# Optimization experiments

Measured on AMD Instinct MI355X. Metric: run time of the kernel, lower is better.

Reference implementation:

```python
import jax, jax.numpy as jnp
import numpy as np

EPS = 1e-5
H = 8  # num_heads

def ln(x, g, b):
    m = x.mean(-1, keepdims=True)
    v = ((x - m) ** 2).mean(-1, keepdims=True)
    return (x - m) / jnp.sqrt(v + EPS) * g + b

def gca(qf, kf, p):
    # Gated cross-modal attention (eval mode, dropout off, mask all-True => no mask)
    (nqg, nqb, nkg, nkb, wq, bq, wk, bk, wv, bv, wo, bo,
     wgp, bgp, g1w, g1b, glng, glnb, g2w, g2b) = p
    B, Sq, _ = qf.shape
    Sk = kf.shape[1]
    E = wq.shape[1]
    D = E // H
    qn = ln(qf, nqg, nqb)
    kn = ln(kf, nkg, nkb)
    q = (qn @ wq + bq).reshape(B, Sq, H, D)
    k = (kn @ wk + bk).reshape(B, Sk, H, D)
    v = (kn @ wv + bv).reshape(B, Sk, H, D)
    scores = jnp.einsum('bqhd,bkhd->bhqk', q, k) * (D ** -0.5)
    w = jax.nn.softmax(scores, axis=-1)          # [B,H,Sq,Sk]
    ctx = jnp.einsum('bhqk,bkhd->bqhd', w, v).reshape(B, Sq, E)
    att = ctx @ wo + bo                          # cross-attention output
    qp = qf @ wgp + bgp                          # query projected for gating
    h = jnp.concatenate([qp, att], axis=-1) @ g1w + g1b
    gate = jax.nn.sigmoid(jax.nn.gelu(ln(h, glng, glnb), approximate=False) @ g2w + g2b)
    return qp + gate * att, w

def ff(x, lng, lnb, w1, b1, w2, b2):
    y = jax.nn.gelu(ln(x, lng, lnb) @ w1 + b1, approximate=False)
    return x + (y @ w2 + b2)

def setup_inputs() -> dict:
    B, Sv, St, Vd, Td, F = 8, 1024, 512, 1024, 768, 512
    keys = iter(jax.random.split(jax.random.key(0), 80))
    def nrm(shape):
        return jax.random.normal(next(keys), shape, jnp.float32) * 0.02
    d = {}
    d['vision_features'] = jax.random.normal(next(keys), (B, Sv, Vd), jnp.float32)
    d['text_features'] = jax.random.normal(next(keys), (B, St, Td), jnp.float32)
    def attn_params(pfx, qd, kd, e):
        d[pfx + 'nq_g'] = jnp.ones(qd); d[pfx + 'nq_b'] = jnp.zeros(qd)
        d[pfx + 'nk_g'] = jnp.ones(kd); d[pfx + 'nk_b'] = jnp.zeros(kd)
        d[pfx + 'wq'] = nrm((qd, e)); d[pfx + 'bq'] = jnp.zeros(e)
        d[pfx + 'wk'] = nrm((kd, e)); d[pfx + 'bk'] = jnp.zeros(e)
        d[pfx + 'wv'] = nrm((kd, e)); d[pfx + 'bv'] = jnp.zeros(e)
        d[pfx + 'wo'] = nrm((e, e)); d[pfx + 'bo'] = jnp.zeros(e)
        d[pfx + 'wgp'] = nrm((qd, e)); d[pfx + 'bgp'] = jnp.zeros(e)
        d[pfx + 'g1w'] = nrm((2 * e, e)); d[pfx + 'g1b'] = jnp.zeros(e)
        d[pfx + 'glng'] = jnp.ones(e); d[pfx + 'glnb'] = jnp.zeros(e)
        d[pfx + 'g2w'] = nrm((e, e)); d[pfx + 'g2b'] = jnp.zeros(e)
    attn_params('t2v_', Td, Vd, F)  # text queries attend to vision
    attn_params('v2t_', Vd, Td, F)  # vision queries attend to text
    for pfx in ('vff_', 'tff_'):
        d[pfx + 'lng'] = jnp.ones(F); d[pfx + 'lnb'] = jnp.zeros(F)
        d[pfx + 'w1'] = nrm((F, 4 * F)); d[pfx + 'b1'] = jnp.zeros(4 * F)
        d[pfx + 'w2'] = nrm((4 * F, F)); d[pfx + 'b2'] = jnp.zeros(F)
    return d

def reference(vision_features, text_features,
              t2v_nq_g, t2v_nq_b, t2v_nk_g, t2v_nk_b, t2v_wq, t2v_bq, t2v_wk, t2v_bk, t2v_wv, t2v_bv, t2v_wo, t2v_bo, t2v_wgp, t2v_bgp, t2v_g1w, t2v_g1b, t2v_glng, t2v_glnb, t2v_g2w, t2v_g2b,
              v2t_nq_g, v2t_nq_b, v2t_nk_g, v2t_nk_b, v2t_wq, v2t_bq, v2t_wk, v2t_bk, v2t_wv, v2t_bv, v2t_wo, v2t_bo, v2t_wgp, v2t_bgp, v2t_g1w, v2t_g1b, v2t_glng, v2t_glnb, v2t_g2w, v2t_g2b,
              vff_lng, vff_lnb, vff_w1, vff_b1, vff_w2, vff_b2,
              tff_lng, tff_lnb, tff_w1, tff_b1, tff_w2, tff_b2):
    t2v_p = (t2v_nq_g, t2v_nq_b, t2v_nk_g, t2v_nk_b, t2v_wq, t2v_bq, t2v_wk, t2v_bk, t2v_wv, t2v_bv, t2v_wo, t2v_bo, t2v_wgp, t2v_bgp, t2v_g1w, t2v_g1b, t2v_glng, t2v_glnb, t2v_g2w, t2v_g2b)
    v2t_p = (v2t_nq_g, v2t_nq_b, v2t_nk_g, v2t_nk_b, v2t_wq, v2t_bq, v2t_wk, v2t_bk, v2t_wv, v2t_bv, v2t_wo, v2t_bo, v2t_wgp, v2t_bgp, v2t_g1w, v2t_g1b, v2t_glng, v2t_glnb, v2t_g2w, v2t_g2b)
    text_att, t2v_w = gca(text_features, vision_features, t2v_p)
    vis_att, v2t_w = gca(vision_features, text_features, v2t_p)
    vision_out = ff(vis_att, vff_lng, vff_lnb, vff_w1, vff_b1, vff_w2, vff_b2)
    text_out = ff(text_att, tff_lng, tff_lnb, tff_w1, tff_b1, tff_w2, tff_b2)
    return (vision_out, text_out, t2v_w, v2t_w)
```

## Files before the change

kernel.cpp:

```cpp
#include <hip/hip_runtime.h>
#include <math.h>


typedef __attribute__((ext_vector_type(8))) short s16x8;
typedef __attribute__((ext_vector_type(4))) float f32x4;
typedef __attribute__((ext_vector_type(4))) unsigned short us4;

__device__ __forceinline__ float gelu_exact(float x) {
  return 0.5f * x * (1.0f + erff(x * 0.70710678118654752f));
}
__device__ __forceinline__ float sigmoidf_(float x) {
  return 1.0f / (1.0f + expf(-x));
}
__device__ __forceinline__ unsigned short f2bf(float f) {
  unsigned int u = __float_as_uint(f);
  u += 0x7fffu + ((u >> 16) & 1u);
  return (unsigned short)(u >> 16);
}

template <bool GELU>
__global__ __launch_bounds__(256) void ln_kernel(
    const float* __restrict__ x, const float* __restrict__ g,
    const float* __restrict__ b, unsigned short* __restrict__ out, int cols) {
  const int row = blockIdx.x;
  const float2* xr = (const float2*)(x + (size_t)row * cols);
  const float2* g2 = (const float2*)g;
  const float2* b2 = (const float2*)b;
  const int n2 = cols >> 1;
  const int tid = threadIdx.x;
  float s = 0.f, ss = 0.f;
  for (int c = tid; c < n2; c += 256) {
    float2 v = xr[c];
    s += v.x + v.y;
    ss += v.x * v.x + v.y * v.y;
  }
#pragma unroll
  for (int off = 32; off; off >>= 1) {
    s += __shfl_down(s, off, 64);
    ss += __shfl_down(ss, off, 64);
  }
  __shared__ float rs[4], rss[4], stat[2];
  const int lane = tid & 63, wid = tid >> 6;
  if (lane == 0) {
    rs[wid] = s;
    rss[wid] = ss;
  }
  __syncthreads();
  if (tid == 0) {
    float ts = rs[0] + rs[1] + rs[2] + rs[3];
    float tss = rss[0] + rss[1] + rss[2] + rss[3];
    float m = ts / (float)cols;
    float var = tss / (float)cols - m * m;
    stat[0] = m;
    stat[1] = 1.0f / sqrtf(var + 1e-5f);
  }
  __syncthreads();
  const float m = stat[0], inv = stat[1];
  ushort2* o2 = (ushort2*)(out + (size_t)row * cols);
  for (int c = tid; c < n2; c += 256) {
    float2 v = xr[c];
    float2 gg = g2[c], bb = b2[c];
    float o0 = (v.x - m) * inv * gg.x + bb.x;
    float o1 = (v.y - m) * inv * gg.y + bb.y;
    if (GELU) {
      o0 = gelu_exact(o0);
      o1 = gelu_exact(o1);
    }
    ushort2 r;
    r.x = f2bf(o0);
    r.y = f2bf(o1);
    o2[c] = r;
  }
}

template <int NIT>
__global__ __launch_bounds__(256) void softmax_kernel(
    float* __restrict__ p, unsigned short* __restrict__ pb) {
  const size_t base = (size_t)blockIdx.x * (NIT * 512);
  float2* pr = (float2*)(p + base);
  ushort2* pb2 = (ushort2*)(pb + base);
  const int tid = threadIdx.x;
  float2 vals[NIT];
  float mx = -1e30f;
#pragma unroll
  for (int i = 0; i < NIT; ++i) {
    vals[i] = pr[tid + i * 256];
    mx = fmaxf(mx, fmaxf(vals[i].x, vals[i].y));
  }
  __shared__ float red[4];
#pragma unroll
  for (int off = 32; off; off >>= 1) mx = fmaxf(mx, __shfl_down(mx, off, 64));
  const int lane = tid & 63, wid = tid >> 6;
  if (lane == 0) red[wid] = mx;
  __syncthreads();
  mx = fmaxf(fmaxf(red[0], red[1]), fmaxf(red[2], red[3]));
  float s = 0.f;
#pragma unroll
  for (int i = 0; i < NIT; ++i) {
    vals[i].x = expf(vals[i].x - mx);
    vals[i].y = expf(vals[i].y - mx);
    s += vals[i].x + vals[i].y;
  }
  __syncthreads();
#pragma unroll
  for (int off = 32; off; off >>= 1) s += __shfl_down(s, off, 64);
  if (lane == 0) red[wid] = s;
  __syncthreads();
  s = red[0] + red[1] + red[2] + red[3];
  const float inv = 1.0f / s;
#pragma unroll
  for (int i = 0; i < NIT; ++i) {
    float2 o;
    o.x = vals[i].x * inv;
    o.y = vals[i].y * inv;
    pr[tid + i * 256] = o;
    ushort2 r;
    r.x = f2bf(o.x);
    r.y = f2bf(o.y);
    pb2[tid + i * 256] = r;
  }
}

__global__ __launch_bounds__(256) void cast_kernel(
    const float* __restrict__ x, unsigned short* __restrict__ o, int n4) {
  const int stride = gridDim.x * 256;
  for (int i = blockIdx.x * 256 + threadIdx.x; i < n4; i += stride) {
    float4 v = ((const float4*)x)[i];
    us4 r = {f2bf(v.x), f2bf(v.y), f2bf(v.z), f2bf(v.w)};
    ((us4*)o)[i] = r;
  }
}

struct TP {
  const float* s[8];
  unsigned short* d[8];
};
__global__ __launch_bounds__(256) void tc_kernel(TP tp, int R, int C) {
  __shared__ unsigned short tile[32][33];
  const float* src = tp.s[blockIdx.z];
  unsigned short* dst = tp.d[blockIdx.z];
  const int r0 = blockIdx.y * 32, c0 = blockIdx.x * 32;
  const int t = threadIdx.x;
  const int tr = t >> 3, tc4 = (t & 7) * 4;
  float4 v = *(const float4*)(src + (size_t)(r0 + tr) * C + c0 + tc4);
  tile[tr][tc4 + 0] = f2bf(v.x);
  tile[tr][tc4 + 1] = f2bf(v.y);
  tile[tr][tc4 + 2] = f2bf(v.z);
  tile[tr][tc4 + 3] = f2bf(v.w);
  __syncthreads();
  us4 o = {tile[tc4 + 0][tr], tile[tc4 + 1][tr], tile[tc4 + 2][tr],
           tile[tc4 + 3][tr]};
  *(us4*)(dst + (size_t)(c0 + tr) * R + r0 + tc4) = o;
}

enum { EPI_B = 0, EPI_BG = 1, EPI_BR = 2, EPI_BGATE = 3, EPI_SC = 4 };

template <int ROWS>
__device__ __forceinline__ void stage_tile(unsigned short (*lds)[40],
                                           const unsigned short* __restrict__ g,
                                           size_t ld) {
  const int t = threadIdx.x;
  const int jr = t & 3;
  const int B0 = (jr < 2) ? (jr * 32) : ((jr - 2) * 32 + 8);
#pragma unroll
  for (int p = 0; p < ROWS / 64; ++p) {
    const int row = (t >> 2) + p * 64;
    uint4 u = *(const uint4*)(g + (size_t)row * ld + jr * 8);
    char* dst = (char*)(&lds[row][0]) + B0;
    *(unsigned long long*)dst = ((const unsigned long long*)&u)[0];
    *(unsigned long long*)(dst + 16) = ((const unsigned long long*)&u)[1];
  }
}

template <int EPI, int OM, int BN, bool CONCAT>
__global__ __launch_bounds__(256) void mm(
    const unsigned short* __restrict__ A0,
    const unsigned short* __restrict__ A1, int lda0, int lda1, int K0, int K,
    const unsigned short* __restrict__ Bt, int ldb,
    const float* __restrict__ bias, const float* __restrict__ X1,
    const float* __restrict__ X2, float* __restrict__ outF,
    unsigned short* __restrict__ outB, int ldc, float scale, size_t aZb,
    size_t aZh, size_t bZb, size_t bZh, size_t cZb, size_t cZh) {
  constexpr int WN = BN / 2;
  constexpr int NJ = WN / 16;
  __shared__ unsigned short As[128][40];
  __shared__ unsigned short Bs[BN][40];
  const int z = blockIdx.z;
  const size_t zb = z >> 3, zh = z & 7;
  const int m0 = blockIdx.y * 128, n0 = blockIdx.x * BN;
  const int t = threadIdx.x;
  const int w = t >> 6, lane = t & 63;
  const int h = lane >> 4, r16 = lane & 15;
  const int wm = w >> 1, wn = w & 1;
  const unsigned short* Ab = A0 + zb * aZb + zh * aZh + (size_t)m0 * lda0;
  const unsigned short* A1b = CONCAT ? (A1 + (size_t)m0 * lda1) : nullptr;
  const unsigned short* Bb = Bt + zb * bZb + zh * bZh + (size_t)n0 * ldb;
  f32x4 acc[4][NJ] = {};
  for (int k0 = 0; k0 < K; k0 += 32) {
    const unsigned short* ag;
    size_t lda;
    if (CONCAT && k0 >= K0) {
      ag = A1b + (k0 - K0);
      lda = (size_t)lda1;
    } else {
      ag = Ab + k0;
      lda = (size_t)lda0;
    }
    stage_tile<128>(As, ag, lda);
    stage_tile<BN>(Bs, Bb + k0, (size_t)ldb);
    __syncthreads();
    const unsigned short* ap = &As[wm * 64 + r16][h * 8];
    const unsigned short* bp = &Bs[wn * WN + r16][h * 8];
    s16x8 av[4], bv[NJ];
#pragma unroll
    for (int i = 0; i < 4; ++i) av[i] = *(const s16x8*)(ap + i * 640);
#pragma unroll
    for (int j = 0; j < NJ; ++j) bv[j] = *(const s16x8*)(bp + j * 640);
#pragma unroll
    for (int i = 0; i < 4; ++i)
#pragma unroll
      for (int j = 0; j < NJ; ++j)
        acc[i][j] = __builtin_amdgcn_mfma_f32_16x16x32_bf16(av[i], bv[j],
                                                            acc[i][j], 0, 0, 0);
    __syncthreads();
  }
  const size_t cz = zb * cZb + zh * cZh;
#pragma unroll
  for (int i = 0; i < 4; ++i) {
    const int rr = m0 + wm * 64 + i * 16 + h * 4;
#pragma unroll
    for (int j = 0; j < NJ; ++j) {
      const int cc = n0 + wn * WN + j * 16 + r16;
      const float bb = (EPI == EPI_SC) ? 0.f : bias[cc];
#pragma unroll
      for (int q = 0; q < 4; ++q) {
        float v = acc[i][j][q];
        v = (EPI == EPI_SC) ? v * scale : v + bb;
        if (EPI == EPI_BG) v = gelu_exact(v);
        const size_t idx = cz + (size_t)(rr + q) * ldc + cc;
        if (EPI == EPI_BR) v = X1[idx] + v;
        if (EPI == EPI_BGATE) v = X1[idx] + sigmoidf_(v) * X2[idx];
        if (OM & 1) outF[idx] = v;
        if (OM & 2) outB[idx] = f2bf(v);
      }
    }
  }
}

extern "C" void kernel_launch(void* const* d_in, const int* in_sizes, int n_in,
                              void* d_out, int out_size, void* d_ws,
                              size_t ws_size, hipStream_t stream) {
  (void)in_sizes;
  (void)n_in;
  (void)out_size;
  (void)ws_size;
  const int B = 8, Sv = 1024, St = 512, Vd = 1024, Td = 768, E = 512;
  auto inf = [&](int i) { return (const float*)d_in[i]; };
  float* out = (float*)d_out;
  char* ws = (char*)d_ws;
  float* out_vis = out;
  float* out_txt = out + 4194304;
  float* w_t2v = out + 6291456;
  float* w_v2t = out + 39845888;

  const size_t BIGo = 0;
  const size_t R1o = 67108864;
  const size_t R2o = R1o + 16777216;
  const size_t R3o = R2o + 16777216;
  const size_t R4o = R3o + 5767168;
  auto U = [&](size_t o) { return (unsigned short*)(ws + o); };
  auto F = [&](size_t o) { return (float*)(ws + o); };

  {
    const int pb = 2;
    const int Sq = St, Sk = Sv, Mq = B * Sq, Mk = B * Sk;
    unsigned short* wq_t = U(R3o + 0);
    unsigned short* wk_t = U(R3o + 786432);
    unsigned short* wv_t = U(R3o + 1835008);
    unsigned short* wo_t = U(R3o + 2883584);
    unsigned short* wgp_t = U(R3o + 3407872);
    unsigned short* g1w_t = U(R3o + 4194304);
    unsigned short* g2w_t = U(R3o + 5242880);
    {
      TP tp{};
      tp.s[0] = inf(pb + 4); tp.d[0] = wq_t;
      tp.s[1] = inf(pb + 12); tp.d[1] = wgp_t;
      tc_kernel<<<dim3(16, 24, 2), 256, 0, stream>>>(tp, 768, 512);
    }
    {
      TP tp{};
      tp.s[0] = inf(pb + 6); tp.d[0] = wk_t;
      tp.s[1] = inf(pb + 8); tp.d[1] = wv_t;
      tp.s[2] = inf(pb + 14); tp.d[2] = g1w_t;
      tc_kernel<<<dim3(16, 32, 3), 256, 0, stream>>>(tp, 1024, 512);
    }
    {
      TP tp{};
      tp.s[0] = inf(pb + 10); tp.d[0] = wo_t;
      tp.s[1] = inf(pb + 18); tp.d[1] = g2w_t;
      tc_kernel<<<dim3(16, 16, 2), 256, 0, stream>>>(tp, 512, 512);
    }
    unsigned short* qn = U(BIGo);
    unsigned short* kn = U(R1o);
    unsigned short* q_bf = U(BIGo + 16777216);
    unsigned short* k_bf = U(BIGo + 25165824);
    float* v_f = F(R2o);
    unsigned short* w_bf = U(BIGo);
    unsigned short* vt = U(R4o);
    unsigned short* ctx_bf = U(R1o);
    float* att_f = F(R2o);
    unsigned short* att_bf = U(BIGo + 50331648);
    unsigned short* txt_bf = U(BIGo);
    float* qp_f = F(R1o + 8388608);
    unsigned short* qp_bf = U(BIGo + 58720256);
    float* h_f = F(BIGo + 16777216);
    unsigned short* hg = U(BIGo);

    ln_kernel<false><<<Mq, 256, 0, stream>>>(inf(1), inf(pb + 0), inf(pb + 1),
                                             qn, Td);
    ln_kernel<false><<<Mk, 256, 0, stream>>>(inf(0), inf(pb + 2), inf(pb + 3),
                                             kn, Vd);
    mm<EPI_B, 2, 64, false><<<dim3(8, 32, 1), 256, 0, stream>>>(
        qn, nullptr, Td, 0, Td, Td, wq_t, Td, inf(pb + 5), nullptr, nullptr,
        nullptr, q_bf, E, 1.f, 0, 0, 0, 0, 0, 0);
    mm<EPI_B, 2, 128, false><<<dim3(4, 64, 1), 256, 0, stream>>>(
        kn, nullptr, Vd, 0, Vd, Vd, wk_t, Vd, inf(pb + 7), nullptr, nullptr,
        nullptr, k_bf, E, 1.f, 0, 0, 0, 0, 0, 0);
    mm<EPI_B, 1, 128, false><<<dim3(4, 64, 1), 256, 0, stream>>>(
        kn, nullptr, Vd, 0, Vd, Vd, wv_t, Vd, inf(pb + 9), nullptr, nullptr,
        v_f, nullptr, E, 1.f, 0, 0, 0, 0, 0, 0);
    mm<EPI_SC, 1, 128, false><<<dim3(Sk / 128, Sq / 128, 64), 256, 0, stream>>>(
        q_bf, nullptr, E, 0, 64, 64, k_bf, E, nullptr, nullptr, nullptr,
        w_t2v, nullptr, Sk, 0.125f, (size_t)Sq * E, 64, (size_t)Sk * E, 64,
        (size_t)8 * Sq * Sk, (size_t)Sq * Sk);
    softmax_kernel<2><<<64 * Sq, 256, 0, stream>>>(w_t2v, w_bf);
    {
      TP tp{};
      for (int i = 0; i < 8; ++i) {
        tp.s[i] = v_f + (size_t)i * Sk * E;
        tp.d[i] = vt + (size_t)i * E * Sk;
      }
      tc_kernel<<<dim3(E / 32, Sk / 32, 8), 256, 0, stream>>>(tp, Sk, E);
    }
    mm<EPI_SC, 2, 64, false><<<dim3(1, Sq / 128, 64), 256, 0, stream>>>(
        w_bf, nullptr, Sk, 0, Sk, Sk, vt, Sk, nullptr, nullptr, nullptr,
        nullptr, ctx_bf, E, 1.f, (size_t)8 * Sq * Sk, (size_t)Sq * Sk,
        (size_t)E * Sk, (size_t)64 * Sk, (size_t)Sq * E, 64);
    mm<EPI_B, 3, 64, false><<<dim3(8, 32, 1), 256, 0, stream>>>(
        ctx_bf, nullptr, E, 0, E, E, wo_t, E, inf(pb + 11), nullptr, nullptr,
        att_f, att_bf, E, 1.f, 0, 0, 0, 0, 0, 0);
    cast_kernel<<<1024, 256, 0, stream>>>(inf(1), txt_bf, Mq * Td / 4);
    mm<EPI_B, 3, 64, false><<<dim3(8, 32, 1), 256, 0, stream>>>(
        txt_bf, nullptr, Td, 0, Td, Td, wgp_t, Td, inf(pb + 13), nullptr,
        nullptr, qp_f, qp_bf, E, 1.f, 0, 0, 0, 0, 0, 0);
    mm<EPI_B, 1, 64, true><<<dim3(8, 32, 1), 256, 0, stream>>>(
        qp_bf, att_bf, E, E, E, 2 * E, g1w_t, 2 * E, inf(pb + 15), nullptr,
        nullptr, h_f, nullptr, E, 1.f, 0, 0, 0, 0, 0, 0);
    ln_kernel<true><<<Mq, 256, 0, stream>>>(h_f, inf(pb + 16), inf(pb + 17),
                                            hg, E);
    mm<EPI_BGATE, 1, 64, false><<<dim3(8, 32, 1), 256, 0, stream>>>(
        hg, nullptr, E, 0, E, E, g2w_t, E, inf(pb + 19), qp_f, att_f, out_txt,
        nullptr, E, 1.f, 0, 0, 0, 0, 0, 0);
  }
  {
    const int pb = 22;
    const int Sq = Sv, Sk = St, Mq = B * Sq, Mk = B * Sk;
    unsigned short* wq_t = U(R3o + 0);
    unsigned short* wk_t = U(R3o + 1048576);
    unsigned short* wv_t = U(R3o + 1835008);
    unsigned short* wo_t = U(R3o + 2621440);
    unsigned short* wgp_t = U(R3o + 3145728);
    unsigned short* g1w_t = U(R3o + 4194304);
    unsigned short* g2w_t = U(R3o + 5242880);
    {
      TP tp{};
      tp.s[0] = inf(pb + 4); tp.d[0] = wq_t;
      tp.s[1] = inf(pb + 12); tp.d[1] = wgp_t;
      tp.s[2] = inf(pb + 14); tp.d[2] = g1w_t;
      tc_kernel<<<dim3(16, 32, 3), 256, 0, stream>>>(tp, 1024, 512);
    }
    {
      TP tp{};
      tp.s[0] = inf(pb + 6); tp.d[0] = wk_t;
      tp.s[1] = inf(pb + 8); tp.d[1] = wv_t;
      tc_kernel<<<dim3(16, 24, 2), 256, 0, stream>>>(tp, 768, 512);
    }
    {
      TP tp{};
      tp.s[0] = inf(pb + 10); tp.d[0] = wo_t;
      tp.s[1] = inf(pb + 18); tp.d[1] = g2w_t;
      tc_kernel<<<dim3(16, 16, 2), 256, 0, stream>>>(tp, 512, 512);
    }
    unsigned short* qn = U(BIGo);
    unsigned short* kn = U(R1o);
    unsigned short* q_bf = U(BIGo + 16777216);
    unsigned short* k_bf = U(BIGo + 25165824);
    float* v_f = F(R2o);
    unsigned short* w_bf = U(BIGo);
    unsigned short* vt = U(R4o);
    unsigned short* ctx_bf = U(R1o);
    float* att_f = F(R2o);
    unsigned short* att_bf = U(BIGo + 50331648);
    unsigned short* vis_bf = U(BIGo);
    float* qp_f = F(R1o);
    unsigned short* qp_bf = U(BIGo + 58720256);
    float* h_f = F(BIGo + 16777216);
    unsigned short* hg = U(BIGo);

    ln_kernel<false><<<Mq, 256, 0, stream>>>(inf(0), inf(pb + 0), inf(pb + 1),
                                             qn, Vd);
    ln_kernel<false><<<Mk, 256, 0, stream>>>(inf(1), inf(pb + 2), inf(pb + 3),
                                             kn, Td);
    mm<EPI_B, 2, 128, false><<<dim3(4, 64, 1), 256, 0, stream>>>(
        qn, nullptr, Vd, 0, Vd, Vd, wq_t, Vd, inf(pb + 5), nullptr, nullptr,
        nullptr, q_bf, E, 1.f, 0, 0, 0, 0, 0, 0);
    mm<EPI_B, 2, 64, false><<<dim3(8, 32, 1), 256, 0, stream>>>(
        kn, nullptr, Td, 0, Td, Td, wk_t, Td, inf(pb + 7), nullptr, nullptr,
        nullptr, k_bf, E, 1.f, 0, 0, 0, 0, 0, 0);
    mm<EPI_B, 1, 64, false><<<dim3(8, 32, 1), 256, 0, stream>>>(
        kn, nullptr, Td, 0, Td, Td, wv_t, Td, inf(pb + 9), nullptr, nullptr,
        v_f, nullptr, E, 1.f, 0, 0, 0, 0, 0, 0);
    mm<EPI_SC, 1, 128, false><<<dim3(Sk / 128, Sq / 128, 64), 256, 0, stream>>>(
        q_bf, nullptr, E, 0, 64, 64, k_bf, E, nullptr, nullptr, nullptr,
        w_v2t, nullptr, Sk, 0.125f, (size_t)Sq * E, 64, (size_t)Sk * E, 64,
        (size_t)8 * Sq * Sk, (size_t)Sq * Sk);
    softmax_kernel<1><<<64 * Sq, 256, 0, stream>>>(w_v2t, w_bf);
    {
      TP tp{};
      for (int i = 0; i < 8; ++i) {
        tp.s[i] = v_f + (size_t)i * Sk * E;
        tp.d[i] = vt + (size_t)i * E * Sk;
      }
      tc_kernel<<<dim3(E / 32, Sk / 32, 8), 256, 0, stream>>>(tp, Sk, E);
    }
    mm<EPI_SC, 2, 64, false><<<dim3(1, Sq / 128, 64), 256, 0, stream>>>(
        w_bf, nullptr, Sk, 0, Sk, Sk, vt, Sk, nullptr, nullptr, nullptr,
        nullptr, ctx_bf, E, 1.f, (size_t)8 * Sq * Sk, (size_t)Sq * Sk,
        (size_t)E * Sk, (size_t)64 * Sk, (size_t)Sq * E, 64);
    mm<EPI_B, 3, 128, false><<<dim3(4, 64, 1), 256, 0, stream>>>(
        ctx_bf, nullptr, E, 0, E, E, wo_t, E, inf(pb + 11), nullptr, nullptr,
        att_f, att_bf, E, 1.f, 0, 0, 0, 0, 0, 0);
    cast_kernel<<<2048, 256, 0, stream>>>(inf(0), vis_bf, Mq * Vd / 4);
    mm<EPI_B, 3, 128, false><<<dim3(4, 64, 1), 256, 0, stream>>>(
        vis_bf, nullptr, Vd, 0, Vd, Vd, wgp_t, Vd, inf(pb + 13), nullptr,
        nullptr, qp_f, qp_bf, E, 1.f, 0, 0, 0, 0, 0, 0);
    mm<EPI_B, 1, 128, true><<<dim3(4, 64, 1), 256, 0, stream>>>(
        qp_bf, att_bf, E, E, E, 2 * E, g1w_t, 2 * E, inf(pb + 15), nullptr,
        nullptr, h_f, nullptr, E, 1.f, 0, 0, 0, 0, 0, 0);
    ln_kernel<true><<<Mq, 256, 0, stream>>>(h_f, inf(pb + 16), inf(pb + 17),
                                            hg, E);
    mm<EPI_BGATE, 1, 128, false><<<dim3(4, 64, 1), 256, 0, stream>>>(
        hg, nullptr, E, 0, E, E, g2w_t, E, inf(pb + 19), qp_f, att_f, out_vis,
        nullptr, E, 1.f, 0, 0, 0, 0, 0, 0);
  }
  {
    unsigned short* vw1_t = U(R3o + 0);
    unsigned short* vw2_t = U(R3o + 2097152);
    unsigned short* tw1_t = U(R3o + 4194304);
    unsigned short* tw2_t = U(R3o + 6291456);
    {
      TP tp{};
      tp.s[0] = inf(44); tp.d[0] = vw1_t;
      tp.s[1] = inf(50); tp.d[1] = tw1_t;
      tc_kernel<<<dim3(64, 16, 2), 256, 0, stream>>>(tp, 512, 2048);
    }
    {
      TP tp{};
      tp.s[0] = inf(46); tp.d[0] = vw2_t;
      tp.s[1] = inf(52); tp.d[1] = tw2_t;
      tc_kernel<<<dim3(16, 64, 2), 256, 0, stream>>>(tp, 2048, 512);
    }
    unsigned short* lnv = U(BIGo);
    unsigned short* y_v = U(BIGo + 8388608);
    unsigned short* lnt = U(BIGo + 41943040);
    unsigned short* y_t = U(BIGo + 46137344);
    ln_kernel<false><<<8192, 256, 0, stream>>>(out_vis, inf(42), inf(43), lnv,
                                               512);
    mm<EPI_BG, 2, 128, false><<<dim3(16, 64, 1), 256, 0, stream>>>(
        lnv, nullptr, 512, 0, 512, 512, vw1_t, 512, inf(45), nullptr, nullptr,
        nullptr, y_v, 2048, 1.f, 0, 0, 0, 0, 0, 0);
    mm<EPI_BR, 1, 128, false><<<dim3(4, 64, 1), 256, 0, stream>>>(
        y_v, nullptr, 2048, 0, 2048, 2048, vw2_t, 2048, inf(47), out_vis,
        nullptr, out_vis, nullptr, 512, 1.f, 0, 0, 0, 0, 0, 0);
    ln_kernel<false><<<4096, 256, 0, stream>>>(out_txt, inf(48), inf(49), lnt,
                                               512);
    mm<EPI_BG, 2, 128, false><<<dim3(16, 32, 1), 256, 0, stream>>>(
        lnt, nullptr, 512, 0, 512, 512, tw1_t, 512, inf(51), nullptr, nullptr,
        nullptr, y_t, 2048, 1.f, 0, 0, 0, 0, 0, 0);
    mm<EPI_BR, 1, 64, false><<<dim3(8, 32, 1), 256, 0, stream>>>(
        y_t, nullptr, 2048, 0, 2048, 2048, tw2_t, 2048, inf(53), out_txt,
        nullptr, out_txt, nullptr, 512, 1.f, 0, 0, 0, 0, 0, 0);
  }
}
```

Measured before the change: 1.209 ms.

## Fuse QK scores with softmax and merge K/V projections with transposed V output

Measured after the change: 1.190 ms. Within noise of the previous version (-1.5%).

```diff
diff --git a/kernel.cpp b/kernel.cpp
--- a/kernel.cpp
+++ b/kernel.cpp
@@ -70,54 +70,6 @@
     r.x = f2bf(o0);
     r.y = f2bf(o1);
     o2[c] = r;
-  }
-}
-
-template <int NIT>
-__global__ __launch_bounds__(256) void softmax_kernel(
-    float* __restrict__ p, unsigned short* __restrict__ pb) {
-  const size_t base = (size_t)blockIdx.x * (NIT * 512);
-  float2* pr = (float2*)(p + base);
-  ushort2* pb2 = (ushort2*)(pb + base);
-  const int tid = threadIdx.x;
-  float2 vals[NIT];
-  float mx = -1e30f;
-#pragma unroll
-  for (int i = 0; i < NIT; ++i) {
-    vals[i] = pr[tid + i * 256];
-    mx = fmaxf(mx, fmaxf(vals[i].x, vals[i].y));
-  }
-  __shared__ float red[4];
-#pragma unroll
-  for (int off = 32; off; off >>= 1) mx = fmaxf(mx, __shfl_down(mx, off, 64));
-  const int lane = tid & 63, wid = tid >> 6;
-  if (lane == 0) red[wid] = mx;
-  __syncthreads();
-  mx = fmaxf(fmaxf(red[0], red[1]), fmaxf(red[2], red[3]));
-  float s = 0.f;
-#pragma unroll
-  for (int i = 0; i < NIT; ++i) {
-    vals[i].x = expf(vals[i].x - mx);
-    vals[i].y = expf(vals[i].y - mx);
-    s += vals[i].x + vals[i].y;
-  }
-  __syncthreads();
-#pragma unroll
-  for (int off = 32; off; off >>= 1) s += __shfl_down(s, off, 64);
-  if (lane == 0) red[wid] = s;
-  __syncthreads();
-  s = red[0] + red[1] + red[2] + red[3];
-  const float inv = 1.0f / s;
-#pragma unroll
-  for (int i = 0; i < NIT; ++i) {
-    float2 o;
-    o.x = vals[i].x * inv;
-    o.y = vals[i].y * inv;
-    pr[tid + i * 256] = o;
-    ushort2 r;
-    r.x = f2bf(o.x);
-    r.y = f2bf(o.y);
-    pb2[tid + i * 256] = r;
   }
 }
 
@@ -153,7 +105,107 @@
   *(us4*)(dst + (size_t)(c0 + tr) * R + r0 + tc4) = o;
 }
 
-enum { EPI_B = 0, EPI_BG = 1, EPI_BR = 2, EPI_BGATE = 3, EPI_SC = 4 };
+template <int SK>
+__global__ __launch_bounds__(256) void attn_sm(
+    const unsigned short* __restrict__ qp, const unsigned short* __restrict__ kp,
+    float* __restrict__ w, unsigned short* __restrict__ wb, int Sq,
+    float scale) {
+  constexpr int TPW = SK / 64;
+  const int z = blockIdx.y, b = z >> 3, h = z & 7;
+  const int q0 = blockIdx.x * 16;
+  const int t = threadIdx.x, wv = t >> 6, lane = t & 63;
+  const int hh = lane >> 4, r16 = lane & 15;
+  const unsigned short* qrow =
+      qp + (size_t)(b * Sq + q0 + r16) * 512 + h * 64 + 4 * hh;
+  s16x8 aq[2];
+#pragma unroll
+  for (int kt = 0; kt < 2; ++kt) {
+    ((unsigned long long*)&aq[kt])[0] =
+        *(const unsigned long long*)(qrow + kt * 32);
+    ((unsigned long long*)&aq[kt])[1] =
+        *(const unsigned long long*)(qrow + kt * 32 + 16);
+  }
+  const unsigned short* kbase = kp + (size_t)b * SK * 512 + h * 64 + 4 * hh;
+  f32x4 sc[TPW];
+#pragma unroll
+  for (int tl = 0; tl < TPW; ++tl) {
+    const unsigned short* krow =
+        kbase + (size_t)(wv * (TPW * 16) + tl * 16 + r16) * 512;
+    s16x8 b0, b1;
+    ((unsigned long long*)&b0)[0] = *(const unsigned long long*)(krow);
+    ((unsigned long long*)&b0)[1] = *(const unsigned long long*)(krow + 16);
+    ((unsigned long long*)&b1)[0] = *(const unsigned long long*)(krow + 32);
+    ((unsigned long long*)&b1)[1] = *(const unsigned long long*)(krow + 48);
+    f32x4 a = {};
+    a = __builtin_amdgcn_mfma_f32_16x16x32_bf16(aq[0], b0, a, 0, 0, 0);
+    a = __builtin_amdgcn_mfma_f32_16x16x32_bf16(aq[1], b1, a, 0, 0, 0);
+    sc[tl] = a * scale;
+  }
+  __shared__ float redM[4][16], redS[4][16];
+  float mx[4], sm[4];
+#pragma unroll
+  for (int q = 0; q < 4; ++q) {
+    float m = sc[0][q];
+#pragma unroll
+    for (int tl = 1; tl < TPW; ++tl) m = fmaxf(m, sc[tl][q]);
+    mx[q] = m;
+  }
+#pragma unroll
+  for (int off = 1; off < 16; off <<= 1)
+#pragma unroll
+    for (int q = 0; q < 4; ++q)
+      mx[q] = fmaxf(mx[q], __shfl_xor(mx[q], off, 64));
+  if (r16 == 0) {
+#pragma unroll
+    for (int q = 0; q < 4; ++q) redM[wv][hh * 4 + q] = mx[q];
+  }
+  __syncthreads();
+#pragma unroll
+  for (int q = 0; q < 4; ++q) {
+    const int rr = hh * 4 + q;
+    mx[q] = fmaxf(fmaxf(redM[0][rr], redM[1][rr]),
+                  fmaxf(redM[2][rr], redM[3][rr]));
+    sm[q] = 0.f;
+  }
+#pragma unroll
+  for (int tl = 0; tl < TPW; ++tl)
+#pragma unroll
+    for (int q = 0; q < 4; ++q) {
+      const float e = expf(sc[tl][q] - mx[q]);
+      sc[tl][q] = e;
+      sm[q] += e;
+    }
+#pragma unroll
+  for (int off = 1; off < 16; off <<= 1)
+#pragma unroll
+    for (int q = 0; q < 4; ++q) sm[q] += __shfl_xor(sm[q], off, 64);
+  if (r16 == 0) {
+#pragma unroll
+    for (int q = 0; q < 4; ++q) redS[wv][hh * 4 + q] = sm[q];
+  }
+  __syncthreads();
+  float inv[4];
+#pragma unroll
+  for (int q = 0; q < 4; ++q) {
+    const int rr = hh * 4 + q;
+    inv[q] = 1.0f / (redS[0][rr] + redS[1][rr] + redS[2][rr] + redS[3][rr]);
+  }
+  float* wrow = w + ((size_t)z * Sq + q0) * SK;
+  unsigned short* wbrow = wb + ((size_t)z * Sq + q0) * SK;
+#pragma unroll
+  for (int tl = 0; tl < TPW; ++tl) {
+    const int col = wv * (TPW * 16) + tl * 16 + r16;
+#pragma unroll
+    for (int q = 0; q < 4; ++q) {
+      const float v = sc[tl][q] * inv[q];
+      const size_t o = (size_t)(hh * 4 + q) * SK + col;
+      wrow[o] = v;
+      wbrow[o] = f2bf(v);
+    }
+  }
+}
+
+enum { EPI_B = 0, EPI_BG = 1, EPI_BR = 2, EPI_BGATE = 3, EPI_SC = 4, EPI_KV = 5 };
 
 template <int ROWS>
 __device__ __forceinline__ void stage_tile(unsigned short (*lds)[40],
@@ -177,10 +229,11 @@
     const unsigned short* __restrict__ A0,
     const unsigned short* __restrict__ A1, int lda0, int lda1, int K0, int K,
     const unsigned short* __restrict__ Bt, int ldb,
-    const float* __restrict__ bias, const float* __restrict__ X1,
-    const float* __restrict__ X2, float* __restrict__ outF,
-    unsigned short* __restrict__ outB, int ldc, float scale, size_t aZb,
-    size_t aZh, size_t bZb, size_t bZh, size_t cZb, size_t cZh) {
+    const float* __restrict__ bias, const float* __restrict__ bias2,
+    const float* __restrict__ X1, const float* __restrict__ X2,
+    float* __restrict__ outF, unsigned short* __restrict__ outB,
+    unsigned short* __restrict__ outT, int ldc, int skShift, float scale,
+    size_t aZb, size_t aZh, size_t bZb, size_t bZh, size_t cZb, size_t cZh) {
   constexpr int WN = BN / 2;
   constexpr int NJ = WN / 16;
   __shared__ unsigned short As[128][40];
@@ -231,17 +284,34 @@
 #pragma unroll
     for (int j = 0; j < NJ; ++j) {
       const int cc = n0 + wn * WN + j * 16 + r16;
-      const float bb = (EPI == EPI_SC) ? 0.f : bias[cc];
-#pragma unroll
-      for (int q = 0; q < 4; ++q) {
-        float v = acc[i][j][q];
-        v = (EPI == EPI_SC) ? v * scale : v + bb;
-        if (EPI == EPI_BG) v = gelu_exact(v);
-        const size_t idx = cz + (size_t)(rr + q) * ldc + cc;
-        if (EPI == EPI_BR) v = X1[idx] + v;
-        if (EPI == EPI_BGATE) v = X1[idx] + sigmoidf_(v) * X2[idx];
-        if (OM & 1) outF[idx] = v;
-        if (OM & 2) outB[idx] = f2bf(v);
+      if (EPI == EPI_KV) {
+        const bool isK = (cc < 512);
+        const float bb = isK ? bias[cc] : bias2[cc - 512];
+#pragma unroll
+        for (int q = 0; q < 4; ++q) {
+          const float v = acc[i][j][q] + bb;
+          const int r = rr + q;
+          if (isK) {
+            outB[(size_t)r * 512 + cc] = f2bf(v);
+          } else {
+            const int b_ = r >> skShift;
+            const int sk = r - (b_ << skShift);
+            outT[(((size_t)b_ * 512 + (cc - 512)) << skShift) + sk] = f2bf(v);
+          }
+        }
+      } else {
+        const float bb = (EPI == EPI_SC) ? 0.f : bias[cc];
+#pragma unroll
+        for (int q = 0; q < 4; ++q) {
+          float v = acc[i][j][q];
+          v = (EPI == EPI_SC) ? v * scale : v + bb;
+          if (EPI == EPI_BG) v = gelu_exact(v);
+          const size_t idx = cz + (size_t)(rr + q) * ldc + cc;
+          if (EPI == EPI_BR) v = X1[idx] + v;
+          if (EPI == EPI_BGATE) v = X1[idx] + sigmoidf_(v) * X2[idx];
+          if (OM & 1) outF[idx] = v;
+          if (OM & 2) outB[idx] = f2bf(v);
+        }
       }
     }
   }
@@ -263,11 +333,13 @@
   float* w_t2v = out + 6291456;
   float* w_v2t = out + 39845888;
 
-  const size_t BIGo = 0;
+  const size_t W0 = 0;
   const size_t R1o = 67108864;
-  const size_t R2o = R1o + 16777216;
-  const size_t R3o = R2o + 16777216;
-  const size_t R4o = R3o + 5767168;
+  const size_t R2o = 83886080;
+  const size_t R3o = 100663296;
+  const size_t R4o = 109051904;
+  const size_t R5o = 117440512;
+  const size_t R6o = 125829120;
   auto U = [&](size_t o) { return (unsigned short*)(ws + o); };
   auto F = [&](size_t o) { return (float*)(ws + o); };
 
@@ -300,71 +372,56 @@
       tp.s[1] = inf(pb + 18); tp.d[1] = g2w_t;
       tc_kernel<<<dim3(16, 16, 2), 256, 0, stream>>>(tp, 512, 512);
     }
-    unsigned short* qn = U(BIGo);
+    unsigned short* qn = U(W0);
     unsigned short* kn = U(R1o);
-    unsigned short* q_bf = U(BIGo + 16777216);
-    unsigned short* k_bf = U(BIGo + 25165824);
-    float* v_f = F(R2o);
-    unsigned short* w_bf = U(BIGo);
+    unsigned short* q_bf = U(R5o);
+    unsigned short* k_bf = U(R6o);
     unsigned short* vt = U(R4o);
+    unsigned short* w_bf = U(W0);
     unsigned short* ctx_bf = U(R1o);
     float* att_f = F(R2o);
-    unsigned short* att_bf = U(BIGo + 50331648);
-    unsigned short* txt_bf = U(BIGo);
+    unsigned short* att_bf = U(W0 + 50331648);
+    unsigned short* txt_bf = U(W0);
     float* qp_f = F(R1o + 8388608);
-    unsigned short* qp_bf = U(BIGo + 58720256);
-    float* h_f = F(BIGo + 16777216);
-    unsigned short* hg = U(BIGo);
+    unsigned short* qp_bf = U(W0 + 58720256);
+    float* h_f = F(W0 + 16777216);
+    unsigned short* hg = U(W0);
 
     ln_kernel<false><<<Mq, 256, 0, stream>>>(inf(1), inf(pb + 0), inf(pb + 1),
                                              qn, Td);
     ln_kernel<false><<<Mk, 256, 0, stream>>>(inf(0), inf(pb + 2), inf(pb + 3),
                                              kn, Vd);
-    mm<EPI_B, 2, 64, false><<<dim3(8, 32, 1), 256, 0, stream>>>(
+    mm<EPI_B, 2, 64, false><<<dim3(8, 32), 256, 0, stream>>>(
         qn, nullptr, Td, 0, Td, Td, wq_t, Td, inf(pb + 5), nullptr, nullptr,
-        nullptr, q_bf, E, 1.f, 0, 0, 0, 0, 0, 0);
-    mm<EPI_B, 2, 128, false><<<dim3(4, 64, 1), 256, 0, stream>>>(
-        kn, nullptr, Vd, 0, Vd, Vd, wk_t, Vd, inf(pb + 7), nullptr, nullptr,
-        nullptr, k_bf, E, 1.f, 0, 0, 0, 0, 0, 0);
-    mm<EPI_B, 1, 128, false><<<dim3(4, 64, 1), 256, 0, stream>>>(
-        kn, nullptr, Vd, 0, Vd, Vd, wv_t, Vd, inf(pb + 9), nullptr, nullptr,
-        v_f, nullptr, E, 1.f, 0, 0, 0, 0, 0, 0);
-    mm<EPI_SC, 1, 128, false><<<dim3(Sk / 128, Sq / 128, 64), 256, 0, stream>>>(
-        q_bf, nullptr, E, 0, 64, 64, k_bf, E, nullptr, nullptr, nullptr,
-        w_t2v, nullptr, Sk, 0.125f, (size_t)Sq * E, 64, (size_t)Sk * E, 64,
-        (size_t)8 * Sq * Sk, (size_t)Sq * Sk);
-    softmax_kernel<2><<<64 * Sq, 256, 0, stream>>>(w_t2v, w_bf);
-    {
-      TP tp{};
-      for (int i = 0; i < 8; ++i) {
-        tp.s[i] = v_f + (size_t)i * Sk * E;
-        tp.d[i] = vt + (size_t)i * E * Sk;
-      }
-      tc_kernel<<<dim3(E / 32, Sk / 32, 8), 256, 0, stream>>>(tp, Sk, E);
-    }
+        nullptr, nullptr, q_bf, nullptr, E, 0, 1.f, 0, 0, 0, 0, 0, 0);
+    mm<EPI_KV, 0, 128, false><<<dim3(8, 64), 256, 0, stream>>>(
+        kn, nullptr, Vd, 0, Vd, Vd, wk_t, Vd, inf(pb + 7), inf(pb + 9),
+        nullptr, nullptr, nullptr, k_bf, vt, 0, 10, 1.f, 0, 0, 0, 0, 0, 0);
+    attn_sm<1024><<<dim3(Sq / 16, 64), 256, 0, stream>>>(q_bf, k_bf, w_t2v,
+                                                         w_bf, Sq, 0.125f);
     mm<EPI_SC, 2, 64, false><<<dim3(1, Sq / 128, 64), 256, 0, stream>>>(
         w_bf, nullptr, Sk, 0, Sk, Sk, vt, Sk, nullptr, nullptr, nullptr,
-        nullptr, ctx_bf, E, 1.f, (size_t)8 * Sq * Sk, (size_t)Sq * Sk,
-        (size_t)E * Sk, (size_t)64 * Sk, (size_t)Sq * E, 64);
-    mm<EPI_B, 3, 64, false><<<dim3(8, 32, 1), 256, 0, stream>>>(
+        nullptr, nullptr, ctx_bf, nullptr, E, 0, 1.f, (size_t)8 * Sq * Sk,
+        (size_t)Sq * Sk, (size_t)E * Sk, (size_t)64 * Sk, (size_t)Sq * E, 64);
+    mm<EPI_B, 3, 64, false><<<dim3(8, 32), 256, 0, stream>>>(
         ctx_bf, nullptr, E, 0, E, E, wo_t, E, inf(pb + 11), nullptr, nullptr,
-        att_f, att_bf, E, 1.f, 0, 0, 0, 0, 0, 0);
+        nullptr, att_f, att_bf, nullptr, E, 0, 1.f, 0, 0, 0, 0, 0, 0);
     cast_kernel<<<1024, 256, 0, stream>>>(inf(1), txt_bf, Mq * Td / 4);
-    mm<EPI_B, 3, 64, false><<<dim3(8, 32, 1), 256, 0, stream>>>(
+    mm<EPI_B, 3, 64, false><<<dim3(8, 32), 256, 0, stream>>>(
         txt_bf, nullptr, Td, 0, Td, Td, wgp_t, Td, inf(pb + 13), nullptr,
-        nullptr, qp_f, qp_bf, E, 1.f, 0, 0, 0, 0, 0, 0);
-    mm<EPI_B, 1, 64, true><<<dim3(8, 32, 1), 256, 0, stream>>>(
+        nullptr, nullptr, qp_f, qp_bf, nullptr, E, 0, 1.f, 0, 0, 0, 0, 0, 0);
+    mm<EPI_B, 1, 64, true><<<dim3(8, 32), 256, 0, stream>>>(
         qp_bf, att_bf, E, E, E, 2 * E, g1w_t, 2 * E, inf(pb + 15), nullptr,
-        nullptr, h_f, nullptr, E, 1.f, 0, 0, 0, 0, 0, 0);
+        nullptr, nullptr, h_f, nullptr, nullptr, E, 0, 1.f, 0, 0, 0, 0, 0, 0);
     ln_kernel<true><<<Mq, 256, 0, stream>>>(h_f, inf(pb + 16), inf(pb + 17),
                                             hg, E);
-    mm<EPI_BGATE, 1, 64, false><<<dim3(8, 32, 1), 256, 0, stream>>>(
-        hg, nullptr, E, 0, E, E, g2w_t, E, inf(pb + 19), qp_f, att_f, out_txt,
-        nullptr, E, 1.f, 0, 0, 0, 0, 0, 0);
+    mm<EPI_BGATE, 1, 64, false><<<dim3(8, 32), 256, 0, stream>>>(
+        hg, nullptr, E, 0, E, E, g2w_t, E, inf(pb + 19), nullptr, qp_f, att_f,
+        out_txt, nullptr, nullptr, E, 0, 1.f, 0, 0, 0, 0, 0, 0);
   }
   {
     const int pb = 22;
-    const int Sq = Sv, Sk = St, Mq = B * Sq, Mk = B * Sk;
+    const int Sq = Sv, Sk = St, Mq = B * Sq, Mk = B * St;
     unsigned short* wq_t = U(R3o + 0);
     unsigned short* wk_t = U(R3o + 1048576);
     unsigned short* wv_t = U(R3o + 1835008);
@@ -391,67 +448,52 @@
       tp.s[1] = inf(pb + 18); tp.d[1] = g2w_t;
       tc_kernel<<<dim3(16, 16, 2), 256, 0, stream>>>(tp, 512, 512);
     }
-    unsigned short* qn = U(BIGo);
+    unsigned short* qn = U(W0);
     unsigned short* kn = U(R1o);
-    unsigned short* q_bf = U(BIGo + 16777216);
-    unsigned short* k_bf = U(BIGo + 25165824);
-    float* v_f = F(R2o);
-    unsigned short* w_bf = U(BIGo);
+    unsigned short* q_bf = U(R5o);
+    unsigned short* k_bf = U(R6o);
     unsigned short* vt = U(R4o);
+    unsigned short* w_bf = U(W0);
     unsigned short* ctx_bf = U(R1o);
     float* att_f = F(R2o);
-    unsigned short* att_bf = U(BIGo + 50331648);
-    unsigned short* vis_bf = U(BIGo);
+    unsigned short* att_bf = U(W0 + 50331648);
+    unsigned short* vis_bf = U(W0);
     float* qp_f = F(R1o);
-    unsigned short* qp_bf = U(BIGo + 58720256);
-    float* h_f = F(BIGo + 16777216);
-    unsigned short* hg = U(BIGo);
+    unsigned short* qp_bf = U(W0 + 58720256);
+    float* h_f = F(W0 + 16777216);
+    unsigned short* hg = U(W0);
 
     ln_kernel<false><<<Mq, 256, 0, stream>>>(inf(0), inf(pb + 0), inf(pb + 1),
                                              qn, Vd);
     ln_kernel<false><<<Mk, 256, 0, stream>>>(inf(1), inf(pb + 2), inf(pb + 3),
                                              kn, Td);
-    mm<EPI_B, 2, 128, false><<<dim3(4, 64, 1), 256, 0, stream>>>(
+    mm<EPI_B, 2, 128, false><<<dim3(4, 64), 256, 0, stream>>>(
         qn, nullptr, Vd, 0, Vd, Vd, wq_t, Vd, inf(pb + 5), nullptr, nullptr,
-        nullptr, q_bf, E, 1.f, 0, 0, 0, 0, 0, 0);
-    mm<EPI_B, 2, 64, false><<<dim3(8, 32, 1), 256, 0, stream>>>(
-        kn, nullptr, Td, 0, Td, Td, wk_t, Td, inf(pb + 7), nullptr, nullptr,
-        nullptr, k_bf, E, 1.f, 0, 0, 0, 0, 0, 0);
-    mm<EPI_B, 1, 64, false><<<dim3(8, 32, 1), 256, 0, stream>>>(
-        kn, nullptr, Td, 0, Td, Td, wv_t, Td, inf(pb + 9), nullptr, nullptr,
-        v_f, nullptr, E, 1.f, 0, 0, 0, 0, 0, 0);
-    mm<EPI_SC, 1, 128, false><<<dim3(Sk / 128, Sq / 128, 64), 256, 0, stream>>>(
-        q_bf, nullptr, E, 0, 64, 64, k_bf, E, nullptr, nullptr, nullptr,
-        w_v2t, nullptr, Sk, 0.125f, (size_t)Sq * E, 64, (size_t)Sk * E, 64,
-        (size_t)8 * Sq * Sk, (size_t)Sq * Sk);
-    softmax_kernel<1><<<64 * Sq, 256, 0, stream>>>(w_v2t, w_bf);
-    {
-      TP tp{};
-      for (int i = 0; i < 8; ++i) {
-        tp.s[i] = v_f + (size_t)i * Sk * E;
-        tp.d[i] = vt + (size_t)i * E * Sk;
-      }
-      tc_kernel<<<dim3(E / 32, Sk / 32, 8), 256, 0, stream>>>(tp, Sk, E);
-    }
+        nullptr, nullptr, q_bf, nullptr, E, 0, 1.f, 0, 0, 0, 0, 0, 0);
+    mm<EPI_KV, 0, 128, false><<<dim3(8, 32), 256, 0, stream>>>(
+        kn, nullptr, Td, 0, Td, Td, wk_t, Td, inf(pb + 7), inf(pb + 9),
+        nullptr, nullptr, nullptr, k_bf, vt, 0, 9, 1.f, 0, 0, 0, 0, 0, 0);
+    attn_sm<512><<<dim3(Sq / 16, 64), 256, 0, stream>>>(q_bf, k_bf, w_v2t,
+                                                        w_bf, Sq, 0.125f);
     mm<EPI_SC, 2, 64, false><<<dim3(1, Sq / 128, 64), 256, 0, stream>>>(
         w_bf, nullptr, Sk, 0, Sk, Sk, vt, Sk, nullptr, nullptr, nullptr,
-        nullptr, ctx_bf, E, 1.f, (size_t)8 * Sq * Sk, (size_t)Sq * Sk,
-        (size_t)E * Sk, (size_t)64 * Sk, (size_t)Sq * E, 64);
-    mm<EPI_B, 3, 128, false><<<dim3(4, 64, 1), 256, 0, stream>>>(
+        nullptr, nullptr, ctx_bf, nullptr, E, 0, 1.f, (size_t)8 * Sq * Sk,
+        (size_t)Sq * Sk, (size_t)E * Sk, (size_t)64 * Sk, (size_t)Sq * E, 64);
+    mm<EPI_B, 3, 128, false><<<dim3(4, 64), 256, 0, stream>>>(
         ctx_bf, nullptr, E, 0, E, E, wo_t, E, inf(pb + 11), nullptr, nullptr,
-        att_f, att_bf, E, 1.f, 0, 0, 0, 0, 0, 0);
+        nullptr, att_f, att_bf, nullptr, E, 0, 1.f, 0, 0, 0, 0, 0, 0);
     cast_kernel<<<2048, 256, 0, stream>>>(inf(0), vis_bf, Mq * Vd / 4);
-    mm<EPI_B, 3, 128, false><<<dim3(4, 64, 1), 256, 0, stream>>>(
+    mm<EPI_B, 3, 128, false><<<dim3(4, 64), 256, 0, stream>>>(
         vis_bf, nullptr, Vd, 0, Vd, Vd, wgp_t, Vd, inf(pb + 13), nullptr,
-        nullptr, qp_f, qp_bf, E, 1.f, 0, 0, 0, 0, 0, 0);
-    mm<EPI_B, 1, 128, true><<<dim3(4, 64, 1), 256, 0, stream>>>(
+        nullptr, nullptr, qp_f, qp_bf, nullptr, E, 0, 1.f, 0, 0, 0, 0, 0, 0);
+    mm<EPI_B, 1, 128, true><<<dim3(4, 64), 256, 0, stream>>>(
         qp_bf, att_bf, E, E, E, 2 * E, g1w_t, 2 * E, inf(pb + 15), nullptr,
-        nullptr, h_f, nullptr, E, 1.f, 0, 0, 0, 0, 0, 0);
+        nullptr, nullptr, h_f, nullptr, nullptr, E, 0, 1.f, 0, 0, 0, 0, 0, 0);
     ln_kernel<true><<<Mq, 256, 0, stream>>>(h_f, inf(pb + 16), inf(pb + 17),
                                             hg, E);
-    mm<EPI_BGATE, 1, 128, false><<<dim3(4, 64, 1), 256, 0, stream>>>(
-        hg, nullptr, E, 0, E, E, g2w_t, E, inf(pb + 19), qp_f, att_f, out_vis,
-        nullptr, E, 1.f, 0, 0, 0, 0, 0, 0);
+    mm<EPI_BGATE, 1, 128, false><<<dim3(4, 64), 256, 0, stream>>>(
+        hg, nullptr, E, 0, E, E, g2w_t, E, inf(pb + 19), nullptr, qp_f, att_f,
+        out_vis, nullptr, nullptr, E, 0, 1.f, 0, 0, 0, 0, 0, 0);
   }
   {
     unsigned short* vw1_t = U(R3o + 0);
@@ -470,25 +512,27 @@
       tp.s[1] = inf(52); tp.d[1] = tw2_t;
       tc_kernel<<<dim3(16, 64, 2), 256, 0, stream>>>(tp, 2048, 512);
     }
-    unsigned short* lnv = U(BIGo);
-    unsigned short* y_v = U(BIGo + 8388608);
-    unsigned short* lnt = U(BIGo + 41943040);
-    unsigned short* y_t = U(BIGo + 46137344);
+    unsigned short* lnv = U(W0);
+    unsigned short* y_v = U(W0 + 8388608);
+    unsigned short* lnt = U(W0 + 41943040);
+    unsigned short* y_t = U(W0 + 46137344);
     ln_kernel<false><<<8192, 256, 0, stream>>>(out_vis, inf(42), inf(43), lnv,
                                                512);
-    mm<EPI_BG, 2, 128, false><<<dim3(16, 64, 1), 256, 0, stream>>>(
+    mm<EPI_BG, 2, 128, false><<<dim3(16, 64), 256, 0, stream>>>(
         lnv, nullptr, 512, 0, 512, 512, vw1_t, 512, inf(45), nullptr, nullptr,
-        nullptr, y_v, 2048, 1.f, 0, 0, 0, 0, 0, 0);
-    mm<EPI_BR, 1, 128, false><<<dim3(4, 64, 1), 256, 0, stream>>>(
-        y_v, nullptr, 2048, 0, 2048, 2048, vw2_t, 2048, inf(47), out_vis,
-        nullptr, out_vis, nullptr, 512, 1.f, 0, 0, 0, 0, 0, 0);
+        nullptr, nullptr, y_v, nullptr, 2048, 0, 1.f, 0, 0, 0, 0, 0, 0);
+    mm<EPI_BR, 1, 128, false><<<dim3(4, 64), 256, 0, stream>>>(
+        y_v, nullptr, 2048, 0, 2048, 2048, vw2_t, 2048, inf(47), nullptr,
+        out_vis, nullptr, out_vis, nullptr, nullptr, 512, 0, 1.f, 0, 0, 0, 0,
+        0, 0);
     ln_kernel<false><<<4096, 256, 0, stream>>>(out_txt, inf(48), inf(49), lnt,
                                                512);
-    mm<EPI_BG, 2, 128, false><<<dim3(16, 32, 1), 256, 0, stream>>>(
+    mm<EPI_BG, 2, 128, false><<<dim3(16, 32), 256, 0, stream>>>(
         lnt, nullptr, 512, 0, 512, 512, tw1_t, 512, inf(51), nullptr, nullptr,
-        nullptr, y_t, 2048, 1.f, 0, 0, 0, 0, 0, 0);
-    mm<EPI_BR, 1, 64, false><<<dim3(8, 32, 1), 256, 0, stream>>>(
-        y_t, nullptr, 2048, 0, 2048, 2048, tw2_t, 2048, inf(53), out_txt,
-        nullptr, out_txt, nullptr, 512, 1.f, 0, 0, 0, 0, 0, 0);
-  }
-}
+        nullptr, nullptr, y_t, nullptr, 2048, 0, 1.f, 0, 0, 0, 0, 0, 0);
+    mm<EPI_BR, 1, 64, false><<<dim3(8, 32), 256, 0, stream>>>(
+        y_t, nullptr, 2048, 0, 2048, 2048, tw2_t, 2048, inf(53), nullptr,
+        out_txt, nullptr, out_txt, nullptr, nullptr, 512, 0, 1.f, 0, 0, 0, 0,
+        0, 0);
+  }
+}
```
